# Performance work log

Measured on AMD Instinct MI355X. Metric: run time of the kernel, lower is better.

The kernel has to match this reference:

```python
import jax, jax.numpy as jnp
import numpy as np

METRIC_SCALE = 0.01  # metric = I + 0.01 * outer(p, p)


def setup_inputs() -> dict:
    key = jax.random.key(0)
    kq, kk = jax.random.split(key)
    query_points = jax.random.normal(kq, (8192, 512), dtype=jnp.float32)
    key_points = jax.random.normal(kk, (8192, 512), dtype=jnp.float32)
    return {"query_points": query_points, "key_points": key_points}


def reference(query_points, key_points):
    # diff_ij = q_i - k_j;  dist^2 under metric (I + c * p p^T) is
    # ||diff||^2 + c * (p . diff)^2 -- avoids materializing [Nq, Nk, d] diffs.
    c = METRIC_SCALE
    qq = jnp.sum(query_points * query_points, axis=-1)          # [Nq]
    kk = jnp.sum(key_points * key_points, axis=-1)              # [Nk]
    qk = jnp.einsum('qd,kd->qk', query_points, key_points)      # [Nq, Nk]
    norm2 = jnp.maximum(qq[:, None] + kk[None, :] - 2.0 * qk, 0.0)
    qdot = qq[:, None] - qk                                     # q_i . (q_i - k_j)
    kdot = qk - kk[None, :]                                     # k_j . (q_i - k_j) (sign irrelevant, squared)
    query_dist = jnp.sqrt(norm2 + c * qdot * qdot)
    key_dist = jnp.sqrt(norm2 + c * kdot * kdot)
    scores = -0.5 * (query_dist + key_dist)
    return jax.nn.softmax(scores, axis=-1)
```

## Files before the change

kernel.cpp:

```cpp
#include <hip/hip_runtime.h>
#include <stdint.h>


#define NQ 8192
#define NK 8192
#define DIM 512
#define CSCALE 0.01f

typedef float f32x4 __attribute__((ext_vector_type(4)));
typedef short s16x8 __attribute__((ext_vector_type(8)));

__device__ __forceinline__ unsigned short f2bf(float x) {
  union { float f; uint32_t u; } c; c.f = x;
  uint32_t u = c.u;
  return (unsigned short)((u + 0x7fffu + ((u >> 16) & 1u)) >> 16);
}

__device__ __forceinline__ s16x8 pack8(f32x4 a, f32x4 b) {
  s16x8 r;
  r[0]=(short)f2bf(a.x); r[1]=(short)f2bf(a.y);
  r[2]=(short)f2bf(a.z); r[3]=(short)f2bf(a.w);
  r[4]=(short)f2bf(b.x); r[5]=(short)f2bf(b.y);
  r[6]=(short)f2bf(b.z); r[7]=(short)f2bf(b.w);
  return r;
}

#define GLOAD_LDS16(g, l)                                                      \
  __builtin_amdgcn_global_load_lds(                                            \
      (const __attribute__((address_space(1))) void*)(g),                      \
      (__attribute__((address_space(3))) void*)(l), 16, 0, 0)

__global__ __launch_bounds__(256) void prep_full_kernel(
    const float* __restrict__ q, const float* __restrict__ k,
    unsigned short* __restrict__ qbf, unsigned short* __restrict__ kbf,
    float* __restrict__ qq, float* __restrict__ kk) {
  int rowg = blockIdx.x * 4 + (threadIdx.x >> 6);
  int lane = threadIdx.x & 63;
  const float* src; unsigned short* dst; float* nrm; int row;
  if (rowg < NQ) { src = q; dst = qbf; nrm = qq; row = rowg; }
  else           { src = k; dst = kbf; nrm = kk; row = rowg - NQ; }
  const float* p = src + (size_t)row * DIM + lane * 8;
  f32x4 a = *(const f32x4*)p;
  f32x4 b = *(const f32x4*)(p + 4);
  float ss = a.x*a.x + a.y*a.y + a.z*a.z + a.w*a.w
           + b.x*b.x + b.y*b.y + b.z*b.z + b.w*b.w;
  *(s16x8*)(dst + (size_t)row * DIM + lane * 8) = pack8(a, b);
#pragma unroll
  for (int mask = 1; mask < 64; mask <<= 1) ss += __shfl_xor(ss, mask, 64);
  if (lane == 0) nrm[row] = ss;
}

__global__ __launch_bounds__(256) void prep_norms_kernel(
    const float* __restrict__ q, const float* __restrict__ k,
    float* __restrict__ qq, float* __restrict__ kk) {
  int rowg = blockIdx.x * 4 + (threadIdx.x >> 6);
  int lane = threadIdx.x & 63;
  const float* src; float* nrm; int row;
  if (rowg < NQ) { src = q; nrm = qq; row = rowg; }
  else           { src = k; nrm = kk; row = rowg - NQ; }
  const float* p = src + (size_t)row * DIM + lane * 8;
  f32x4 a = *(const f32x4*)p;
  f32x4 b = *(const f32x4*)(p + 4);
  float ss = a.x*a.x + a.y*a.y + a.z*a.z + a.w*a.w
           + b.x*b.x + b.y*b.y + b.z*b.z + b.w*b.w;
#pragma unroll
  for (int mask = 1; mask < 64; mask <<= 1) ss += __shfl_xor(ss, mask, 64);
  if (lane == 0) nrm[row] = ss;
}

__device__ __forceinline__ void score_epilogue(
    const f32x4 acc[4][4], const float* __restrict__ qq,
    const float* __restrict__ kk, float* __restrict__ S,
    int m0, int n0, int wr, int wc, int quad, int lcol) {
  float kkv[4];
#pragma unroll
  for (int ni = 0; ni < 4; ++ni) kkv[ni] = kk[n0 + wc * 64 + ni * 16 + lcol];
#pragma unroll
  for (int mi = 0; mi < 4; ++mi) {
    const int ibase = m0 + wr * 64 + mi * 16 + quad * 4;
    float qqv[4];
#pragma unroll
    for (int r = 0; r < 4; ++r) qqv[r] = qq[ibase + r];
#pragma unroll
    for (int ni = 0; ni < 4; ++ni) {
      const int col = n0 + wc * 64 + ni * 16 + lcol;
#pragma unroll
      for (int r = 0; r < 4; ++r) {
        float qkv = acc[mi][ni][r];
        float n2 = fmaxf(qqv[r] + kkv[ni] - 2.f * qkv, 0.f);
        float qd = qqv[r] - qkv;
        float kd = qkv - kkv[ni];
        float s = -0.5f * (sqrtf(n2 + CSCALE * qd * qd) +
                           sqrtf(n2 + CSCALE * kd * kd));
        S[(size_t)(ibase + r) * NK + col] = s;
      }
    }
  }
}

__global__ __launch_bounds__(256) void gemm_fast_kernel(
    const unsigned short* __restrict__ qbf, const unsigned short* __restrict__ kbf,
    const float* __restrict__ qq, const float* __restrict__ kk,
    float* __restrict__ S) {
  __shared__ unsigned short lA[128 * 32];
  __shared__ unsigned short lB[128 * 32];
  const int tid = threadIdx.x;
  const int m0 = blockIdx.y * 128;
  const int n0 = blockIdx.x * 128;
  const int wave = tid >> 6, lane = tid & 63;
  const int wr = wave >> 1, wc = wave & 1;
  const int quad = lane >> 4, lcol = lane & 15;

  const unsigned short* ga = qbf + (size_t)(m0 + (tid >> 2)) * DIM + (tid & 3) * 8;
  const unsigned short* gb = kbf + (size_t)(n0 + (tid >> 2)) * DIM + (tid & 3) * 8;
  char* la0 = (char*)lA + wave * 1024;
  char* lb0 = (char*)lB + wave * 1024;

  f32x4 acc[4][4];
#pragma unroll
  for (int mi = 0; mi < 4; ++mi)
#pragma unroll
    for (int ni = 0; ni < 4; ++ni) acc[mi][ni] = f32x4{0.f, 0.f, 0.f, 0.f};

  const s16x8* lA8 = (const s16x8*)lA;
  const s16x8* lB8 = (const s16x8*)lB;
  const int arow = wr * 64 + lcol;
  const int brow = wc * 64 + lcol;

  for (int kt = 0; kt < DIM / 32; ++kt) {
    const int ko = kt * 32;
    GLOAD_LDS16(ga + ko, la0);
    GLOAD_LDS16(ga + ko + 64 * DIM, la0 + 4096);
    GLOAD_LDS16(gb + ko, lb0);
    GLOAD_LDS16(gb + ko + 64 * DIM, lb0 + 4096);
    __syncthreads();
    s16x8 af[4], bfr[4];
#pragma unroll
    for (int mi = 0; mi < 4; ++mi) af[mi] = lA8[(arow + mi * 16) * 4 + quad];
#pragma unroll
    for (int ni = 0; ni < 4; ++ni) bfr[ni] = lB8[(brow + ni * 16) * 4 + quad];
#pragma unroll
    for (int mi = 0; mi < 4; ++mi)
#pragma unroll
      for (int ni = 0; ni < 4; ++ni)
        acc[mi][ni] = __builtin_amdgcn_mfma_f32_16x16x32_bf16(
            af[mi], bfr[ni], acc[mi][ni], 0, 0, 0);
    __syncthreads();
  }
  score_epilogue(acc, qq, kk, S, m0, n0, wr, wc, quad, lcol);
}

__global__ __launch_bounds__(256) void gemm_safe_kernel(
    const float* __restrict__ q, const float* __restrict__ k,
    const float* __restrict__ qq, const float* __restrict__ kk,
    float* __restrict__ S) {
  __shared__ unsigned short lA[128 * 32];
  __shared__ unsigned short lB[128 * 32];
  const int tid = threadIdx.x;
  const int m0 = blockIdx.y * 128;
  const int n0 = blockIdx.x * 128;
  const int wave = tid >> 6, lane = tid & 63;
  const int wr = wave >> 1, wc = wave & 1;
  const int quad = lane >> 4, lcol = lane & 15;

  const float* gaf = q + (size_t)(m0 + (tid >> 1)) * DIM + (tid & 1) * 16;
  const float* gbf = k + (size_t)(n0 + (tid >> 1)) * DIM + (tid & 1) * 16;
  unsigned short* wA = lA + (tid >> 1) * 32 + (tid & 1) * 16;
  unsigned short* wB = lB + (tid >> 1) * 32 + (tid & 1) * 16;

  f32x4 acc[4][4];
#pragma unroll
  for (int mi = 0; mi < 4; ++mi)
#pragma unroll
    for (int ni = 0; ni < 4; ++ni) acc[mi][ni] = f32x4{0.f, 0.f, 0.f, 0.f};

  const s16x8* lA8 = (const s16x8*)lA;
  const s16x8* lB8 = (const s16x8*)lB;
  const int arow = wr * 64 + lcol;
  const int brow = wc * 64 + lcol;

  for (int kt = 0; kt < DIM / 32; ++kt) {
    const float* pa = gaf + kt * 32;
    const float* pb = gbf + kt * 32;
    f32x4 a0 = *(const f32x4*)(pa), a1 = *(const f32x4*)(pa + 4);
    f32x4 a2 = *(const f32x4*)(pa + 8), a3 = *(const f32x4*)(pa + 12);
    f32x4 b0 = *(const f32x4*)(pb), b1 = *(const f32x4*)(pb + 4);
    f32x4 b2 = *(const f32x4*)(pb + 8), b3 = *(const f32x4*)(pb + 12);
    *(s16x8*)wA = pack8(a0, a1);
    *(s16x8*)(wA + 8) = pack8(a2, a3);
    *(s16x8*)wB = pack8(b0, b1);
    *(s16x8*)(wB + 8) = pack8(b2, b3);
    __syncthreads();
    s16x8 af[4], bfr[4];
#pragma unroll
    for (int mi = 0; mi < 4; ++mi) af[mi] = lA8[(arow + mi * 16) * 4 + quad];
#pragma unroll
    for (int ni = 0; ni < 4; ++ni) bfr[ni] = lB8[(brow + ni * 16) * 4 + quad];
#pragma unroll
    for (int mi = 0; mi < 4; ++mi)
#pragma unroll
      for (int ni = 0; ni < 4; ++ni)
        acc[mi][ni] = __builtin_amdgcn_mfma_f32_16x16x32_bf16(
            af[mi], bfr[ni], acc[mi][ni], 0, 0, 0);
    __syncthreads();
  }
  score_epilogue(acc, qq, kk, S, m0, n0, wr, wc, quad, lcol);
}

__global__ __launch_bounds__(256) void rowsoftmax_kernel(float* __restrict__ S) {
  __shared__ float red[8];
  const int t = threadIdx.x;
  const int wave = t >> 6, lane = t & 63;
  float* Srow = S + (size_t)blockIdx.x * NK;
  f32x4 v[8];
  float m = -1e30f;
#pragma unroll
  for (int j = 0; j < 8; ++j) {
    v[j] = *(const f32x4*)(Srow + j * 1024 + t * 4);
    m = fmaxf(m, fmaxf(fmaxf(v[j].x, v[j].y), fmaxf(v[j].z, v[j].w)));
  }
#pragma unroll
  for (int mask = 1; mask < 64; mask <<= 1) m = fmaxf(m, __shfl_xor(m, mask, 64));
  if (lane == 0) red[wave] = m;
  __syncthreads();
  m = fmaxf(fmaxf(red[0], red[1]), fmaxf(red[2], red[3]));
  float s = 0.f;
#pragma unroll
  for (int j = 0; j < 8; ++j) {
    v[j].x = __expf(v[j].x - m);
    v[j].y = __expf(v[j].y - m);
    v[j].z = __expf(v[j].z - m);
    v[j].w = __expf(v[j].w - m);
    s += (v[j].x + v[j].y) + (v[j].z + v[j].w);
  }
#pragma unroll
  for (int mask = 1; mask < 64; mask <<= 1) s += __shfl_xor(s, mask, 64);
  if (lane == 0) red[4 + wave] = s;
  __syncthreads();
  float z = 1.0f / ((red[4] + red[5]) + (red[6] + red[7]));
#pragma unroll
  for (int j = 0; j < 8; ++j) {
    v[j].x *= z; v[j].y *= z; v[j].z *= z; v[j].w *= z;
    *(f32x4*)(Srow + j * 1024 + t * 4) = v[j];
  }
}

extern "C" void kernel_launch(void* const* d_in, const int* in_sizes, int n_in,
                              void* d_out, int out_size, void* d_ws, size_t ws_size,
                              hipStream_t stream) {
  const float* q = (const float*)d_in[0];
  const float* k = (const float*)d_in[1];
  float* S = (float*)d_out;
  char* ws = (char*)d_ws;

  const bool fast = ws_size >= (size_t)16842752;
  if (fast) {
    unsigned short* qbf = (unsigned short*)(ws);
    unsigned short* kbf = (unsigned short*)(ws + 8388608);
    float* qq = (float*)(ws + 16777216);
    float* kk = (float*)(ws + 16777216 + 32768);
    prep_full_kernel<<<4096, 256, 0, stream>>>(q, k, qbf, kbf, qq, kk);
    gemm_fast_kernel<<<dim3(64, 64), 256, 0, stream>>>(qbf, kbf, qq, kk, S);
  } else {
    float* qq = (float*)(ws);
    float* kk = (float*)(ws + 32768);
    prep_norms_kernel<<<4096, 256, 0, stream>>>(q, k, qq, kk);
    gemm_safe_kernel<<<dim3(64, 64), 256, 0, stream>>>(q, k, qq, kk, S);
  }
  rowsoftmax_kernel<<<NQ, 256, 0, stream>>>(S);
}
```

Baseline: 492.0 us.

## Fuse exp into GEMM epilogue, store bf16 exponentials, single-pass normalize

Adds a path in which the GEMM epilogue computes exp(score) directly, with no max subtraction since the scores are always non-positive. It rounds the results to bf16, stages them through per-wave LDS for coalesced 16-byte stores, and writes them into a large workspace buffer. A lighter row kernel then sums the bf16 values and writes the normalized fp32 output, replacing the fp32 score round trip and the full softmax. This roughly halves the intermediate traffic, at the cost of bf16 precision in the output. The path is taken only when the workspace is at least about 151 MB.

```diff
diff --git a/kernel.cpp b/kernel.cpp
--- a/kernel.cpp
+++ b/kernel.cpp
@@ -9,11 +9,17 @@
 
 typedef float f32x4 __attribute__((ext_vector_type(4)));
 typedef short s16x8 __attribute__((ext_vector_type(8)));
+typedef unsigned short u16x4 __attribute__((ext_vector_type(4)));
 
 __device__ __forceinline__ unsigned short f2bf(float x) {
   union { float f; uint32_t u; } c; c.f = x;
   uint32_t u = c.u;
   return (unsigned short)((u + 0x7fffu + ((u >> 16) & 1u)) >> 16);
+}
+
+__device__ __forceinline__ float bf2f(unsigned short h) {
+  union { uint32_t u; float f; } c; c.u = ((uint32_t)h) << 16;
+  return c.f;
 }
 
 __device__ __forceinline__ s16x8 pack8(f32x4 a, f32x4 b) {
@@ -68,6 +74,124 @@
   if (lane == 0) nrm[row] = ss;
 }
 
+__device__ __forceinline__ float score_fn(float qkv, float qqv, float kkv) {
+  float n2 = fmaxf(qqv + kkv - 2.f * qkv, 0.f);
+  float qd = qqv - qkv;
+  float kd = qkv - kkv;
+  return -0.5f * (sqrtf(n2 + CSCALE * qd * qd) +
+                  sqrtf(n2 + CSCALE * kd * kd));
+}
+
+__global__ __launch_bounds__(256) void gemm_exp_kernel(
+    const unsigned short* __restrict__ qbf, const unsigned short* __restrict__ kbf,
+    const float* __restrict__ qq, const float* __restrict__ kk,
+    unsigned short* __restrict__ E) {
+  __shared__ unsigned short lA[128 * 32];
+  __shared__ unsigned short lB[128 * 32];
+  __shared__ alignas(16) unsigned short lT[4][16 * 80];
+  const int tid = threadIdx.x;
+  const int m0 = blockIdx.y * 128;
+  const int n0 = blockIdx.x * 128;
+  const int wave = tid >> 6, lane = tid & 63;
+  const int wr = wave >> 1, wc = wave & 1;
+  const int quad = lane >> 4, lcol = lane & 15;
+
+  const unsigned short* ga = qbf + (size_t)(m0 + (tid >> 2)) * DIM + (tid & 3) * 8;
+  const unsigned short* gb = kbf + (size_t)(n0 + (tid >> 2)) * DIM + (tid & 3) * 8;
+  char* la0 = (char*)lA + wave * 1024;
+  char* lb0 = (char*)lB + wave * 1024;
+
+  f32x4 acc[4][4];
+#pragma unroll
+  for (int mi = 0; mi < 4; ++mi)
+#pragma unroll
+    for (int ni = 0; ni < 4; ++ni) acc[mi][ni] = f32x4{0.f, 0.f, 0.f, 0.f};
+
+  const s16x8* lA8 = (const s16x8*)lA;
+  const s16x8* lB8 = (const s16x8*)lB;
+  const int arow = wr * 64 + lcol;
+  const int brow = wc * 64 + lcol;
+
+  for (int kt = 0; kt < DIM / 32; ++kt) {
+    const int ko = kt * 32;
+    GLOAD_LDS16(ga + ko, la0);
+    GLOAD_LDS16(ga + ko + 64 * DIM, la0 + 4096);
+    GLOAD_LDS16(gb + ko, lb0);
+    GLOAD_LDS16(gb + ko + 64 * DIM, lb0 + 4096);
+    __syncthreads();
+    s16x8 af[4], bfr[4];
+#pragma unroll
+    for (int mi = 0; mi < 4; ++mi) af[mi] = lA8[(arow + mi * 16) * 4 + quad];
+#pragma unroll
+    for (int ni = 0; ni < 4; ++ni) bfr[ni] = lB8[(brow + ni * 16) * 4 + quad];
+#pragma unroll
+    for (int mi = 0; mi < 4; ++mi)
+#pragma unroll
+      for (int ni = 0; ni < 4; ++ni)
+        acc[mi][ni] = __builtin_amdgcn_mfma_f32_16x16x32_bf16(
+            af[mi], bfr[ni], acc[mi][ni], 0, 0, 0);
+    __syncthreads();
+  }
+
+  unsigned short* tw = &lT[wave][0];
+  float kkv[4];
+#pragma unroll
+  for (int ni = 0; ni < 4; ++ni) kkv[ni] = kk[n0 + wc * 64 + ni * 16 + lcol];
+#pragma unroll
+  for (int mi = 0; mi < 4; ++mi) {
+    const int ibase = m0 + wr * 64 + mi * 16 + quad * 4;
+    float qqv[4];
+#pragma unroll
+    for (int r = 0; r < 4; ++r) qqv[r] = qq[ibase + r];
+#pragma unroll
+    for (int ni = 0; ni < 4; ++ni)
+#pragma unroll
+      for (int r = 0; r < 4; ++r) {
+        float e = __expf(score_fn(acc[mi][ni][r], qqv[r], kkv[ni]));
+        tw[(quad * 4 + r) * 80 + ((ni ^ quad) * 16 + lcol)] = f2bf(e);
+      }
+#pragma unroll
+    for (int j = 0; j < 2; ++j) {
+      const int row16 = (lane >> 3) + j * 8;
+      const int g = (lane & 7) >> 1;
+      const int off = row16 * 80 + ((g ^ (row16 >> 2)) * 16) + (lane & 1) * 8;
+      s16x8 vv = *(const s16x8*)(tw + off);
+      const int rowg = m0 + wr * 64 + mi * 16 + row16;
+      *(s16x8*)(E + (size_t)rowg * NK + n0 + wc * 64 + (lane & 7) * 8) = vv;
+    }
+  }
+}
+
+__global__ __launch_bounds__(256) void rowsum_scale_kernel(
+    const unsigned short* __restrict__ E, float* __restrict__ out) {
+  __shared__ float red[4];
+  const int t = threadIdx.x;
+  const int wave = t >> 6, lane = t & 63;
+  const unsigned short* Erow = E + (size_t)blockIdx.x * NK;
+  float* Orow = out + (size_t)blockIdx.x * NK;
+  u16x4 ev[8];
+  float s = 0.f;
+#pragma unroll
+  for (int j = 0; j < 8; ++j) {
+    ev[j] = *(const u16x4*)(Erow + j * 1024 + t * 4);
+    s += (bf2f(ev[j][0]) + bf2f(ev[j][1])) + (bf2f(ev[j][2]) + bf2f(ev[j][3]));
+  }
+#pragma unroll
+  for (int mask = 1; mask < 64; mask <<= 1) s += __shfl_xor(s, mask, 64);
+  if (lane == 0) red[wave] = s;
+  __syncthreads();
+  float z = 1.0f / ((red[0] + red[1]) + (red[2] + red[3]));
+#pragma unroll
+  for (int j = 0; j < 8; ++j) {
+    f32x4 v;
+    v.x = bf2f(ev[j][0]) * z;
+    v.y = bf2f(ev[j][1]) * z;
+    v.z = bf2f(ev[j][2]) * z;
+    v.w = bf2f(ev[j][3]) * z;
+    *(f32x4*)(Orow + j * 1024 + t * 4) = v;
+  }
+}
+
 __device__ __forceinline__ void score_epilogue(
     const f32x4 acc[4][4], const float* __restrict__ qq,
     const float* __restrict__ kk, float* __restrict__ S,
@@ -85,15 +209,8 @@
     for (int ni = 0; ni < 4; ++ni) {
       const int col = n0 + wc * 64 + ni * 16 + lcol;
 #pragma unroll
-      for (int r = 0; r < 4; ++r) {
-        float qkv = acc[mi][ni][r];
-        float n2 = fmaxf(qqv[r] + kkv[ni] - 2.f * qkv, 0.f);
-        float qd = qqv[r] - qkv;
-        float kd = qkv - kkv[ni];
-        float s = -0.5f * (sqrtf(n2 + CSCALE * qd * qd) +
-                           sqrtf(n2 + CSCALE * kd * kd));
-        S[(size_t)(ibase + r) * NK + col] = s;
-      }
+      for (int r = 0; r < 4; ++r)
+        S[(size_t)(ibase + r) * NK + col] = score_fn(acc[mi][ni][r], qqv[r], kkv[ni]);
     }
   }
 }
@@ -110,23 +227,19 @@
   const int wave = tid >> 6, lane = tid & 63;
   const int wr = wave >> 1, wc = wave & 1;
   const int quad = lane >> 4, lcol = lane & 15;
-
   const unsigned short* ga = qbf + (size_t)(m0 + (tid >> 2)) * DIM + (tid & 3) * 8;
   const unsigned short* gb = kbf + (size_t)(n0 + (tid >> 2)) * DIM + (tid & 3) * 8;
   char* la0 = (char*)lA + wave * 1024;
   char* lb0 = (char*)lB + wave * 1024;
-
   f32x4 acc[4][4];
 #pragma unroll
   for (int mi = 0; mi < 4; ++mi)
 #pragma unroll
     for (int ni = 0; ni < 4; ++ni) acc[mi][ni] = f32x4{0.f, 0.f, 0.f, 0.f};
-
   const s16x8* lA8 = (const s16x8*)lA;
   const s16x8* lB8 = (const s16x8*)lB;
   const int arow = wr * 64 + lcol;
   const int brow = wc * 64 + lcol;
-
   for (int kt = 0; kt < DIM / 32; ++kt) {
     const int ko = kt * 32;
     GLOAD_LDS16(ga + ko, la0);
@@ -162,23 +275,19 @@
   const int wave = tid >> 6, lane = tid & 63;
   const int wr = wave >> 1, wc = wave & 1;
   const int quad = lane >> 4, lcol = lane & 15;
-
   const float* gaf = q + (size_t)(m0 + (tid >> 1)) * DIM + (tid & 1) * 16;
   const float* gbf = k + (size_t)(n0 + (tid >> 1)) * DIM + (tid & 1) * 16;
   unsigned short* wA = lA + (tid >> 1) * 32 + (tid & 1) * 16;
   unsigned short* wB = lB + (tid >> 1) * 32 + (tid & 1) * 16;
-
   f32x4 acc[4][4];
 #pragma unroll
   for (int mi = 0; mi < 4; ++mi)
 #pragma unroll
     for (int ni = 0; ni < 4; ++ni) acc[mi][ni] = f32x4{0.f, 0.f, 0.f, 0.f};
-
   const s16x8* lA8 = (const s16x8*)lA;
   const s16x8* lB8 = (const s16x8*)lB;
   const int arow = wr * 64 + lcol;
   const int brow = wc * 64 + lcol;
-
   for (int kt = 0; kt < DIM / 32; ++kt) {
     const float* pa = gaf + kt * 32;
     const float* pb = gbf + kt * 32;
@@ -253,19 +362,28 @@
   float* S = (float*)d_out;
   char* ws = (char*)d_ws;
 
-  const bool fast = ws_size >= (size_t)16842752;
-  if (fast) {
+  if (ws_size >= (size_t)151126016) {
+    unsigned short* qbf = (unsigned short*)(ws);
+    unsigned short* kbf = (unsigned short*)(ws + 8388608);
+    float* qq = (float*)(ws + 16777216);
+    float* kk = (float*)(ws + 16777216 + 32768);
+    unsigned short* E = (unsigned short*)(ws + 16908288);
+    prep_full_kernel<<<4096, 256, 0, stream>>>(q, k, qbf, kbf, qq, kk);
+    gemm_exp_kernel<<<dim3(64, 64), 256, 0, stream>>>(qbf, kbf, qq, kk, E);
+    rowsum_scale_kernel<<<NQ, 256, 0, stream>>>(E, S);
+  } else if (ws_size >= (size_t)16842752) {
     unsigned short* qbf = (unsigned short*)(ws);
     unsigned short* kbf = (unsigned short*)(ws + 8388608);
     float* qq = (float*)(ws + 16777216);
     float* kk = (float*)(ws + 16777216 + 32768);
     prep_full_kernel<<<4096, 256, 0, stream>>>(q, k, qbf, kbf, qq, kk);
     gemm_fast_kernel<<<dim3(64, 64), 256, 0, stream>>>(qbf, kbf, qq, kk, S);
+    rowsoftmax_kernel<<<NQ, 256, 0, stream>>>(S);
   } else {
     float* qq = (float*)(ws);
     float* kk = (float*)(ws + 32768);
     prep_norms_kernel<<<4096, 256, 0, stream>>>(q, k, qq, kk);
     gemm_safe_kernel<<<dim3(64, 64), 256, 0, stream>>>(q, k, qq, kk, S);
-  }
-  rowsoftmax_kernel<<<NQ, 256, 0, stream>>>(S);
-}
+    rowsoftmax_kernel<<<NQ, 256, 0, stream>>>(S);
+  }
+}
```

Measured after the change: 466.8 us. 1.05x faster.
